# Kernel optimization log

Hardware: AMD Instinct MI355X
Metric: run time of the kernel (lower is better)

## Reference

```python
import jax, jax.numpy as jnp
import numpy as np

B, S, D, H, L, V = 2, 1024, 1024, 16, 8, 50257
HD = D // H
FF = 4 * D
EPS = 1e-5


def setup_inputs() -> dict:
    key = jax.random.key(0)
    ks = jax.random.split(key, 16)
    s = 0.02
    return {
        "idx": jax.random.randint(ks[0], (B, S), 0, V, dtype=jnp.int32),
        "tok_emb": jax.random.normal(ks[1], (V, D), jnp.float32) * s,
        "pos_emb": jax.random.normal(ks[2], (S, D), jnp.float32) * s,
        "qkv_w": jax.random.normal(ks[3], (L, 3 * D, D), jnp.float32) * s,
        "proj_w": jax.random.normal(ks[4], (L, D, D), jnp.float32) * s,
        "proj_b": jnp.zeros((L, D), jnp.float32),
        "ln1_s": jnp.ones((L, D), jnp.float32),
        "ln1_b": jnp.zeros((L, D), jnp.float32),
        "fc1_w": jax.random.normal(ks[5], (L, FF, D), jnp.float32) * s,
        "fc1_b": jnp.zeros((L, FF), jnp.float32),
        "fc2_w": jax.random.normal(ks[6], (L, D, FF), jnp.float32) * s,
        "fc2_b": jnp.zeros((L, D), jnp.float32),
        "ln2_s": jnp.ones((L, D), jnp.float32),
        "ln2_b": jnp.zeros((L, D), jnp.float32),
        "lnf_s": jnp.ones((D,), jnp.float32),
        "lnf_b": jnp.zeros((D,), jnp.float32),
        "head_w": jax.random.normal(ks[7], (V, D), jnp.float32) * s,
        "head_b": jnp.zeros((V,), jnp.float32),
    }


def _layer_norm(x, scale, bias):
    mu = jnp.mean(x, axis=-1, keepdims=True)
    var = jnp.mean(jnp.square(x - mu), axis=-1, keepdims=True)
    return (x - mu) * jax.lax.rsqrt(var + EPS) * scale + bias


def _attention(x, qkv_w, proj_w, proj_b, causal):
    b, s, d = x.shape
    qkv = jnp.einsum("bsd,ed->bse", x, qkv_w)            # [B,S,3D]
    qkv = qkv.reshape(b, s, H, 3 * HD)                    # per-head interleaved q,k,v
    q, k, v = jnp.split(qkv, 3, axis=-1)                  # each [B,S,H,HD]
    scale = HD ** -0.5
    scores = jnp.einsum("bqhd,bkhd->bhqk", q, k) * scale  # [B,H,S,S]
    scores = jnp.where(causal, scores, -jnp.inf)
    probs = jax.nn.softmax(scores, axis=-1)
    out = jnp.einsum("bhqk,bkhd->bqhd", probs, v).reshape(b, s, d)
    return out @ proj_w.T + proj_b


def reference(idx, tok_emb, pos_emb, qkv_w, proj_w, proj_b, ln1_s, ln1_b,
              fc1_w, fc1_b, fc2_w, fc2_b, ln2_s, ln2_b, lnf_s, lnf_b,
              head_w, head_b):
    s = idx.shape[1]
    causal = jnp.tril(jnp.ones((s, s), dtype=bool))
    x = tok_emb[idx] + pos_emb[None, :s]                  # [B,S,D]
    for l in range(L):
        h = _layer_norm(x, ln1_s[l], ln1_b[l])
        x = x + _attention(h, qkv_w[l], proj_w[l], proj_b[l], causal)
        h = _layer_norm(x, ln2_s[l], ln2_b[l])
        h = jax.nn.relu(h @ fc1_w[l].T + fc1_b[l]) @ fc2_w[l].T + fc2_b[l]
        x = x + h
    x = _layer_norm(x, lnf_s, lnf_b)
    logits = x @ head_w.T + head_b                        # [B,S,V]
    return logits
```

## Files before the change

kernel.cpp:

```cpp
#include <hip/hip_runtime.h>
#include <hip/hip_bf16.h>
#include <math.h>

#define B_  2
#define S_  1024
#define D_  1024
#define H_  16
#define HD_ 64
#define L_  8
#define FF_ 4096
#define V_  50257
#define M_  (B_ * S_)
#define EPS_ 1e-5f

typedef __attribute__((ext_vector_type(8))) short short8;
typedef __attribute__((ext_vector_type(4))) float f32x4;

__device__ __forceinline__ unsigned short f2bf(float f) {
  union { float f; uint32_t u; } c; c.f = f;
  uint32_t r = (c.u + 0x7FFFu + ((c.u >> 16) & 1u)) >> 16;
  return (unsigned short)r;
}
__device__ __forceinline__ void gll16(const unsigned short* g, unsigned short* lds) {
  __builtin_amdgcn_global_load_lds(
      (const __attribute__((address_space(1))) void*)g,
      (__attribute__((address_space(3))) void*)lds, 16, 0, 0);
}

__global__ __launch_bounds__(256) void embed_kernel(
    const int* __restrict__ idx, const float* __restrict__ tok,
    const float* __restrict__ pos, float* __restrict__ x) {
  int i = blockIdx.x * 256 + threadIdx.x;
  int m = i >> 8;
  int d4 = i & 255;
  int s = m & (S_ - 1);
  int t = idx[m];
  float4 tv = ((const float4*)(tok + (size_t)t * D_))[d4];
  float4 pv = ((const float4*)(pos + (size_t)s * D_))[d4];
  float4 o;
  o.x = tv.x + pv.x; o.y = tv.y + pv.y; o.z = tv.z + pv.z; o.w = tv.w + pv.w;
  ((float4*)(x + (size_t)m * D_))[d4] = o;
}

__global__ __launch_bounds__(256) void cvt_bf16_kernel(
    const float* __restrict__ in, unsigned short* __restrict__ out, int n4) {
  int i = blockIdx.x * 256 + threadIdx.x;
  int stride = gridDim.x * 256;
  for (; i < n4; i += stride) {
    float4 v = ((const float4*)in)[i];
    ushort4 o;
    o.x = f2bf(v.x); o.y = f2bf(v.y); o.z = f2bf(v.z); o.w = f2bf(v.w);
    ((ushort4*)out)[i] = o;
  }
}

__global__ __launch_bounds__(256) void cvt4_kernel(
    const float* __restrict__ s0, const float* __restrict__ s1,
    const float* __restrict__ s2, const float* __restrict__ s3,
    unsigned short* __restrict__ d0, unsigned short* __restrict__ d1,
    unsigned short* __restrict__ d2, unsigned short* __restrict__ d3,
    int n0, int n1, int n2, int n3) {
  int total = n0 + n1 + n2 + n3;
  for (int i = blockIdx.x * 256 + threadIdx.x; i < total; i += gridDim.x * 256) {
    const float* s; unsigned short* d; int j = i;
    if (j < n0)              { s = s0; d = d0; }
    else if ((j -= n0) < n1) { s = s1; d = d1; }
    else if ((j -= n1) < n2) { s = s2; d = d2; }
    else                     { j -= n2; s = s3; d = d3; }
    float4 v = ((const float4*)s)[j];
    ushort4 o;
    o.x = f2bf(v.x); o.y = f2bf(v.y); o.z = f2bf(v.z); o.w = f2bf(v.w);
    ((ushort4*)d)[j] = o;
  }
}

__device__ __forceinline__ float block_sum256(float v, float* red) {
  #pragma unroll
  for (int o = 32; o > 0; o >>= 1) v += __shfl_xor(v, o);
  int w = threadIdx.x >> 6;
  __syncthreads();
  if ((threadIdx.x & 63) == 0) red[w] = v;
  __syncthreads();
  return red[0] + red[1] + red[2] + red[3];
}

__global__ __launch_bounds__(256) void layernorm_kernel(
    const float* __restrict__ x, const float* __restrict__ sc,
    const float* __restrict__ bi, unsigned short* __restrict__ out) {
  __shared__ float red[4];
  int row = blockIdx.x;
  float4 v = ((const float4*)(x + (size_t)row * D_))[threadIdx.x];
  float sum = block_sum256(v.x + v.y + v.z + v.w, red);
  float mu = sum * (1.0f / D_);
  float dx = v.x - mu, dy = v.y - mu, dz = v.z - mu, dw = v.w - mu;
  float sq = block_sum256(dx*dx + dy*dy + dz*dz + dw*dw, red);
  float r = rsqrtf(sq * (1.0f / D_) + EPS_);
  int c = threadIdx.x * 4;
  float4 s4 = *(const float4*)(sc + c);
  float4 b4 = *(const float4*)(bi + c);
  ushort4 o;
  o.x = f2bf(dx * r * s4.x + b4.x);
  o.y = f2bf(dy * r * s4.y + b4.y);
  o.z = f2bf(dz * r * s4.z + b4.z);
  o.w = f2bf(dw * r * s4.w + b4.w);
  ((ushort4*)(out + (size_t)row * D_))[threadIdx.x] = o;
}

__global__ __launch_bounds__(256) void reduce_ln_kernel(
    const float* __restrict__ parts, const float* __restrict__ bias,
    float* __restrict__ x, const float* __restrict__ sc,
    const float* __restrict__ bi, unsigned short* __restrict__ h) {
  __shared__ float red[4];
  int row = blockIdx.x;
  int i = row * 256 + threadIdx.x;
  float4 v = ((const float4*)x)[i];
  float4 bb = ((const float4*)bias)[threadIdx.x];
  v.x += bb.x; v.y += bb.y; v.z += bb.z; v.w += bb.w;
  #pragma unroll
  for (int z = 0; z < 4; ++z) {
    float4 p = ((const float4*)(parts + (size_t)z * M_ * D_))[i];
    v.x += p.x; v.y += p.y; v.z += p.z; v.w += p.w;
  }
  ((float4*)x)[i] = v;
  float sum = block_sum256(v.x + v.y + v.z + v.w, red);
  float mu = sum * (1.0f / D_);
  float dx = v.x - mu, dy = v.y - mu, dz = v.z - mu, dw = v.w - mu;
  float sq = block_sum256(dx*dx + dy*dy + dz*dz + dw*dw, red);
  float r = rsqrtf(sq * (1.0f / D_) + EPS_);
  int c = threadIdx.x * 4;
  float4 s4 = *(const float4*)(sc + c);
  float4 b4 = *(const float4*)(bi + c);
  ushort4 o;
  o.x = f2bf(dx * r * s4.x + b4.x);
  o.y = f2bf(dy * r * s4.y + b4.y);
  o.z = f2bf(dz * r * s4.z + b4.z);
  o.w = f2bf(dw * r * s4.w + b4.w);
  ((ushort4*)(h + (size_t)row * D_))[threadIdx.x] = o;
}

#define BM 128
#define BN 128
#define BKg 64

template<bool BIAS, bool RELU, bool OUTBF16>
__global__ __launch_bounds__(256) void gemm_mfma(
    const unsigned short* __restrict__ A, const unsigned short* __restrict__ W,
    const float* __restrict__ bias, void* __restrict__ Cout,
    int M, int N, int K, int lda, int ldc, size_t zstride, int nbx) {
  __shared__ unsigned short As[BM * BKg];
  __shared__ unsigned short Bs[BN * BKg];

  int nwg = gridDim.x;
  int bid = blockIdx.x;
  int q = nwg >> 3, r = nwg & 7;
  int xcd = bid & 7, sub = bid >> 3;
  int swz = (xcd < r ? xcd * (q + 1) : r * (q + 1) + (xcd - r) * q) + sub;
  int by = swz / nbx, bx = swz % nbx;
  int bm = by * BM, bn = bx * BN;

  const size_t Koff = (size_t)blockIdx.y * K;
  const unsigned short* Ab = A + Koff;
  const unsigned short* Wb = W + Koff;

  const int tid = threadIdx.x;
  const int l = tid & 63, w = tid >> 6;
  const int wm = (w >> 1) * 64, wn = (w & 1) * 64;
  const int lr = l >> 3;
  const int lc = (l & 7) << 3;

  const unsigned short* asrc[4];
  const unsigned short* bsrc[4];
  unsigned short* adst[4];
  unsigned short* bdst[4];
  #pragma unroll
  for (int i = 0; i < 4; ++i) {
    int rowa = i * 32 + w * 8;
    asrc[i] = Ab + (size_t)(bm + rowa + lr) * lda + lc;
    adst[i] = As + rowa * BKg;
    int gn = bn + rowa + lr; if (gn >= N) gn = N - 1;
    bsrc[i] = Wb + (size_t)gn * lda + lc;
    bdst[i] = Bs + rowa * BKg;
  }

  f32x4 acc[4][4] = {};
  for (int k0 = 0; k0 < K; k0 += BKg) {
    __syncthreads();
    #pragma unroll
    for (int i = 0; i < 4; ++i) {
      gll16(asrc[i] + k0, adst[i]);
      gll16(bsrc[i] + k0, bdst[i]);
    }
    __syncthreads();
    short8 af[2][4], bfr[2][4];
    #pragma unroll
    for (int ks = 0; ks < 2; ++ks)
      #pragma unroll
      for (int i = 0; i < 4; ++i) {
        af[ks][i]  = *(const short8*)(As + (wm + i * 16 + (l & 15)) * BKg + ks * 32 + (l >> 4) * 8);
        bfr[ks][i] = *(const short8*)(Bs + (wn + i * 16 + (l & 15)) * BKg + ks * 32 + (l >> 4) * 8);
      }
    #pragma unroll
    for (int ks = 0; ks < 2; ++ks)
      #pragma unroll
      for (int i = 0; i < 4; ++i)
        #pragma unroll
        for (int j = 0; j < 4; ++j)
          acc[i][j] = __builtin_amdgcn_mfma_f32_16x16x32_bf16(af[ks][i], bfr[ks][j], acc[i][j], 0, 0, 0);
  }

  const size_t zoff = (size_t)blockIdx.y * zstride;
  const int er = (l >> 4) * 4;
  const int ec = l & 15;
  #pragma unroll
  for (int j = 0; j < 4; ++j) {
    int col = bn + wn + j * 16 + ec;
    if (col < N) {
      float bv = BIAS ? bias[col] : 0.f;
      #pragma unroll
      for (int i = 0; i < 4; ++i) {
        #pragma unroll
        for (int rr = 0; rr < 4; ++rr) {
          int row = bm + wm + i * 16 + er + rr;
          float v = acc[i][j][rr] + bv;
          if (RELU) v = fmaxf(v, 0.f);
          if (OUTBF16) ((unsigned short*)Cout + zoff)[(size_t)row * ldc + col] = f2bf(v);
          else         ((float*)Cout + zoff)[(size_t)row * ldc + col] = v;
        }
      }
    }
  }
}

__global__ __launch_bounds__(256) void attn_mfma_kernel(
    const unsigned short* __restrict__ qkv, unsigned short* __restrict__ out) {
  __shared__ unsigned short Kl[128 * 72];
  __shared__ unsigned short Vt[64 * 136];
  __shared__ unsigned short Pl[4 * 16 * 136];
  const int h = blockIdx.y, b = blockIdx.z;
  const int tile = b ? blockIdx.x : (15 - blockIdx.x);
  const int q0 = tile * 64;
  const int nt = (q0 + 191) >> 7;
  const int tid = threadIdx.x;
  const int l = tid & 63, wid = tid >> 6;
  const int g = l >> 4, m15 = l & 15;
  const size_t rs = 3 * D_;
  const unsigned short* base = qkv + (size_t)(b * S_) * rs + h * (3 * HD_);
  const int sd = wid * 16;
  unsigned short* Pw = Pl + wid * 16 * 136;

  const unsigned short* qp = base + (size_t)(q0 + wid * 16 + m15) * rs + g * 8;
  short8 qf0 = *(const short8*)(qp);
  short8 qf1 = *(const short8*)(qp + 32);
  f32x4 acc_o[4] = {};
  float mrun[4] = {-INFINITY, -INFINITY, -INFINITY, -INFINITY};
  float ssum[4] = {0.f, 0.f, 0.f, 0.f};

  short8 kA0, kA1, kB0, kB1, vA0, vA1, vB0, vB1;
  {
    const unsigned short* r0 = base + (size_t)l * rs + HD_ + sd;
    const unsigned short* r1 = r0 + 64 * rs;
    kA0 = *(const short8*)(r0);       kA1 = *(const short8*)(r0 + 8);
    vA0 = *(const short8*)(r0 + HD_); vA1 = *(const short8*)(r0 + HD_ + 8);
    kB0 = *(const short8*)(r1);       kB1 = *(const short8*)(r1 + 8);
    vB0 = *(const short8*)(r1 + HD_); vB1 = *(const short8*)(r1 + HD_ + 8);
  }

  for (int kt = 0; kt < nt; ++kt) {
    const int k128 = kt << 7;
    __syncthreads();
    *(short8*)(Kl + l * 72 + sd) = kA0;
    *(short8*)(Kl + l * 72 + sd + 8) = kA1;
    *(short8*)(Kl + (64 + l) * 72 + sd) = kB0;
    *(short8*)(Kl + (64 + l) * 72 + sd + 8) = kB1;
    #pragma unroll
    for (int e = 0; e < 8; ++e) {
      Vt[(sd + e) * 136 + l] = (unsigned short)vA0[e];
      Vt[(sd + 8 + e) * 136 + l] = (unsigned short)vA1[e];
      Vt[(sd + e) * 136 + 64 + l] = (unsigned short)vB0[e];
      Vt[(sd + 8 + e) * 136 + 64 + l] = (unsigned short)vB1[e];
    }
    __syncthreads();
    if (kt + 1 < nt) {
      const unsigned short* r0 = base + (size_t)(k128 + 128 + l) * rs + HD_ + sd;
      const unsigned short* r1 = r0 + 64 * rs;
      kA0 = *(const short8*)(r0);       kA1 = *(const short8*)(r0 + 8);
      vA0 = *(const short8*)(r0 + HD_); vA1 = *(const short8*)(r0 + HD_ + 8);
      kB0 = *(const short8*)(r1);       kB1 = *(const short8*)(r1 + 8);
      vB0 = *(const short8*)(r1 + HD_); vB1 = *(const short8*)(r1 + HD_ + 8);
    }

    f32x4 sc8[8] = {};
    __builtin_amdgcn_s_setprio(1);
    #pragma unroll
    for (int j = 0; j < 8; ++j) {
      short8 kf0 = *(const short8*)(Kl + (j * 16 + m15) * 72 + g * 8);
      short8 kf1 = *(const short8*)(Kl + (j * 16 + m15) * 72 + 32 + g * 8);
      sc8[j] = __builtin_amdgcn_mfma_f32_16x16x32_bf16(qf0, kf0, sc8[j], 0, 0, 0);
      sc8[j] = __builtin_amdgcn_mfma_f32_16x16x32_bf16(qf1, kf1, sc8[j], 0, 0, 0);
    }
    __builtin_amdgcn_s_setprio(0);

    const bool lastt = (kt == nt - 1);
    #pragma unroll
    for (int rr = 0; rr < 4; ++rr) {
      const int qrow = q0 + wid * 16 + g * 4 + rr;
      float sv[8];
      #pragma unroll
      for (int j = 0; j < 8; ++j) {
        sv[j] = sc8[j][rr] * 0.125f;
        if (lastt && (k128 + j * 16 + m15 > qrow)) sv[j] = -1e30f;
      }
      float mx = sv[0];
      #pragma unroll
      for (int j = 1; j < 8; ++j) mx = fmaxf(mx, sv[j]);
      mx = fmaxf(mx, __shfl_xor(mx, 1));
      mx = fmaxf(mx, __shfl_xor(mx, 2));
      mx = fmaxf(mx, __shfl_xor(mx, 4));
      mx = fmaxf(mx, __shfl_xor(mx, 8));
      float mn = fmaxf(mrun[rr], mx);
      float corr = __expf(mrun[rr] - mn);
      mrun[rr] = mn;
      float ts = 0.f;
      #pragma unroll
      for (int j = 0; j < 8; ++j) {
        float p = __expf(sv[j] - mn);
        ts += p;
        Pw[(g * 4 + rr) * 136 + j * 16 + m15] = f2bf(p);
      }
      ts += __shfl_xor(ts, 1); ts += __shfl_xor(ts, 2);
      ts += __shfl_xor(ts, 4); ts += __shfl_xor(ts, 8);
      ssum[rr] = ssum[rr] * corr + ts;
      #pragma unroll
      for (int j = 0; j < 4; ++j) acc_o[j][rr] *= corr;
    }

    short8 pa[4];
    #pragma unroll
    for (int ks = 0; ks < 4; ++ks)
      pa[ks] = *(const short8*)(Pw + m15 * 136 + ks * 32 + g * 8);
    __builtin_amdgcn_s_setprio(1);
    #pragma unroll
    for (int j = 0; j < 4; ++j) {
      #pragma unroll
      for (int ks = 0; ks < 4; ++ks) {
        short8 vb = *(const short8*)(Vt + (j * 16 + m15) * 136 + ks * 32 + g * 8);
        acc_o[j] = __builtin_amdgcn_mfma_f32_16x16x32_bf16(pa[ks], vb, acc_o[j], 0, 0, 0);
      }
    }
    __builtin_amdgcn_s_setprio(0);
  }

  #pragma unroll
  for (int rr = 0; rr < 4; ++rr) {
    const int qrow = q0 + wid * 16 + g * 4 + rr;
    float inv = 1.0f / ssum[rr];
    #pragma unroll
    for (int j = 0; j < 4; ++j)
      out[(size_t)(b * S_ + qrow) * D_ + h * HD_ + j * 16 + m15] =
          f2bf(acc_o[j][rr] * inv);
  }
}

static inline void cvt(const float* src, unsigned short* dst, size_t n, hipStream_t s) {
  int n4 = (int)(n / 4);
  int blocks = (n4 + 255) / 256;
  if (blocks > 2048) blocks = 2048;
  cvt_bf16_kernel<<<blocks, 256, 0, s>>>(src, dst, n4);
}

extern "C" void kernel_launch(void* const* d_in, const int* in_sizes, int n_in,
                              void* d_out, int out_size, void* d_ws, size_t ws_size,
                              hipStream_t stream) {
  const int*   idx    = (const int*)d_in[0];
  const float* tok    = (const float*)d_in[1];
  const float* pos    = (const float*)d_in[2];
  const float* qkv_w  = (const float*)d_in[3];
  const float* proj_w = (const float*)d_in[4];
  const float* proj_b = (const float*)d_in[5];
  const float* ln1_s  = (const float*)d_in[6];
  const float* ln1_b  = (const float*)d_in[7];
  const float* fc1_w  = (const float*)d_in[8];
  const float* fc1_b  = (const float*)d_in[9];
  const float* fc2_w  = (const float*)d_in[10];
  const float* fc2_b  = (const float*)d_in[11];
  const float* ln2_s  = (const float*)d_in[12];
  const float* ln2_b  = (const float*)d_in[13];
  const float* lnf_s  = (const float*)d_in[14];
  const float* lnf_b  = (const float*)d_in[15];
  const float* head_w = (const float*)d_in[16];
  const float* head_b = (const float*)d_in[17];
  float* out = (float*)d_out;

  char* wsb = (char*)d_ws;
  float*          x      = (float*)(wsb);
  unsigned short* h      = (unsigned short*)(wsb + (8u << 20));
  unsigned short* qkvb   = (unsigned short*)(wsb + (12u << 20));
  unsigned short* attnb  = (unsigned short*)(wsb + (24u << 20));
  unsigned short* ff     = (unsigned short*)(wsb + (28u << 20));
  unsigned short* wq     = (unsigned short*)(wsb + (44u << 20));
  unsigned short* wp     = (unsigned short*)(wsb + (50u << 20));
  unsigned short* w1     = (unsigned short*)(wsb + (52u << 20));
  unsigned short* w2     = (unsigned short*)(wsb + (60u << 20));
  float*          parts  = (float*)(wsb + (68u << 20));
  unsigned short* hw     = (unsigned short*)(wsb + (100u << 20));

  embed_kernel<<<M_ * D_ / 4 / 256, 256, 0, stream>>>(idx, tok, pos, x);
  layernorm_kernel<<<M_, 256, 0, stream>>>(x, ln1_s, ln1_b, h);

  for (int l = 0; l < L_; ++l) {
    cvt4_kernel<<<2048, 256, 0, stream>>>(
        qkv_w + (size_t)l * 3 * D_ * D_, proj_w + (size_t)l * D_ * D_,
        fc1_w + (size_t)l * FF_ * D_, fc2_w + (size_t)l * D_ * FF_,
        wq, wp, w1, w2,
        3 * D_ * D_ / 4, D_ * D_ / 4, FF_ * D_ / 4, D_ * FF_ / 4);
    gemm_mfma<false, false, true><<<dim3(24 * 16, 1), 256, 0, stream>>>(
        h, wq, nullptr, qkvb, M_, 3 * D_, D_, D_, 3 * D_, 0, 24);
    attn_mfma_kernel<<<dim3(16, H_, B_), 256, 0, stream>>>(qkvb, attnb);
    gemm_mfma<false, false, false><<<dim3(8 * 16, 4), 256, 0, stream>>>(
        attnb, wp, nullptr, parts, M_, D_, 256, D_, D_, (size_t)M_ * D_, 8);
    reduce_ln_kernel<<<M_, 256, 0, stream>>>(
        parts, proj_b + l * D_, x, ln2_s + l * D_, ln2_b + l * D_, h);
    gemm_mfma<true, true, true><<<dim3(32 * 16, 1), 256, 0, stream>>>(
        h, w1, fc1_b + l * FF_, ff, M_, FF_, D_, D_, FF_, 0, 32);
    gemm_mfma<false, false, false><<<dim3(8 * 16, 4), 256, 0, stream>>>(
        ff, w2, nullptr, parts, M_, D_, 1024, FF_, D_, (size_t)M_ * D_, 8);
    const float* ns = (l == L_ - 1) ? lnf_s : ln1_s + (l + 1) * D_;
    const float* nb = (l == L_ - 1) ? lnf_b : ln1_b + (l + 1) * D_;
    reduce_ln_kernel<<<M_, 256, 0, stream>>>(
        parts, fc2_b + l * D_, x, ns, nb, h);
  }

  for (int c0 = 0; c0 < V_; c0 += 8192) {
    int nc = V_ - c0 < 8192 ? V_ - c0 : 8192;
    cvt(head_w + (size_t)c0 * D_, hw, (size_t)nc * D_, stream);
    int nbx = (nc + BN - 1) / BN, nby = M_ / BM;
    gemm_mfma<true, false, false><<<dim3(nbx * nby, 1), 256, 0, stream>>>(
        h, hw, head_b + c0, out + c0, M_, nc, D_, D_, V_, 0, nbx);
  }
}
```

Baseline: 1.884 ms.

## Add specialized 256x256 LM-head GEMM kernel and hoist weight conversion out of the layer loop

Replaces the chunked LM-head path, which converted the head weights 8192 rows at a time and ran one generic GEMM per chunk, with a single dedicated 256x256-tile, 512-thread MFMA kernel. That kernel double-buffers LDS through global_load_lds, uses a swizzled LDS layout, interleaves staging with MFMA phases, raises wave priority around the MFMAs, and swizzles block order. The head weights are padded to a multiple of 256 rows with zeros so the kernel needs no bounds checks on loads. All layer weights are converted to bf16 in a few bulk conversions up front instead of once per layer. The cost is a much larger workspace (about 380 MB) and 128 KB of dynamic LDS per block, which relies on 160 KB LDS per CU.

```diff
diff --git a/kernel.cpp b/kernel.cpp
--- a/kernel.cpp
+++ b/kernel.cpp
@@ -10,8 +10,10 @@
 #define L_  8
 #define FF_ 4096
 #define V_  50257
+#define VP_ 50432
 #define M_  (B_ * S_)
 #define EPS_ 1e-5f
+#define NT_ 16
 
 typedef __attribute__((ext_vector_type(8))) short short8;
 typedef __attribute__((ext_vector_type(4))) float f32x4;
@@ -54,24 +56,10 @@
   }
 }
 
-__global__ __launch_bounds__(256) void cvt4_kernel(
-    const float* __restrict__ s0, const float* __restrict__ s1,
-    const float* __restrict__ s2, const float* __restrict__ s3,
-    unsigned short* __restrict__ d0, unsigned short* __restrict__ d1,
-    unsigned short* __restrict__ d2, unsigned short* __restrict__ d3,
-    int n0, int n1, int n2, int n3) {
-  int total = n0 + n1 + n2 + n3;
-  for (int i = blockIdx.x * 256 + threadIdx.x; i < total; i += gridDim.x * 256) {
-    const float* s; unsigned short* d; int j = i;
-    if (j < n0)              { s = s0; d = d0; }
-    else if ((j -= n0) < n1) { s = s1; d = d1; }
-    else if ((j -= n1) < n2) { s = s2; d = d2; }
-    else                     { j -= n2; s = s3; d = d3; }
-    float4 v = ((const float4*)s)[j];
-    ushort4 o;
-    o.x = f2bf(v.x); o.y = f2bf(v.y); o.z = f2bf(v.z); o.w = f2bf(v.w);
-    ((ushort4*)d)[j] = o;
-  }
+__global__ __launch_bounds__(256) void pad_head_kernel(unsigned short* __restrict__ w) {
+  int i = blockIdx.x * 256 + threadIdx.x;
+  ushort4 z; z.x = 0; z.y = 0; z.z = 0; z.w = 0;
+  ((ushort4*)(w + (size_t)V_ * D_))[i] = z;
 }
 
 __device__ __forceinline__ float block_sum256(float v, float* red) {
@@ -229,6 +217,137 @@
       }
     }
   }
+}
+
+__global__ __launch_bounds__(512, 2) void gemm_head_8p(
+    const unsigned short* __restrict__ A, const unsigned short* __restrict__ W,
+    const float* __restrict__ bias, float* __restrict__ C) {
+  extern __shared__ unsigned short lds[];
+
+  const int nbq = 197;
+  int bid = blockIdx.x;
+  int swz = (bid & 7) * nbq + (bid >> 3);
+  const int bm = (swz & 7) * 256;
+  const int bn = (swz >> 3) * 256;
+
+  const int tid = threadIdx.x;
+  const int l = tid & 63;
+  const int wid = tid >> 6;
+  const int wm = wid >> 2, wn = wid & 3;
+  const int m15 = l & 15, g = l >> 4;
+
+  const int srow = tid >> 2;
+  const int scol = ((tid & 3) * 8) ^ (((tid >> 5) & 1) << 4);
+  const unsigned short* Asrc = A + (size_t)(bm + srow) * 1024 + scol;
+  const unsigned short* Bsrc = W + (size_t)(bn + srow) * 1024 + scol;
+  unsigned short* ldsA = lds + tid * 8;
+  unsigned short* ldsB = lds + 16384 + tid * 8;
+
+  const int arow = wm * 128 + m15;
+  const int asw = (g * 8) ^ (((arow >> 3) & 1) << 4);
+  const unsigned short* aRd = lds + arow * 32 + asw;
+  const int brow = wn * 64 + m15;
+  const int bsw = (g * 8) ^ (((brow >> 3) & 1) << 4);
+  const unsigned short* bRd = lds + 16384 + brow * 32 + bsw;
+
+#define STG_(tt, kh, s) do {                                                          \
+    gll16(Asrc + (size_t)(s) * 131072 + (tt) * 64 + (kh) * 32,                        \
+          ldsA + (((tt) & 1) << 15) + ((kh) << 13) + ((s) << 12));                    \
+    gll16(Bsrc + (size_t)(s) * 131072 + (tt) * 64 + (kh) * 32,                        \
+          ldsB + (((tt) & 1) << 15) + ((kh) << 13) + ((s) << 12));                    \
+  } while (0)
+#define BAR_() do { __builtin_amdgcn_s_barrier(); __builtin_amdgcn_sched_barrier(0); } while (0)
+
+  f32x4 acc[8][4] = {};
+
+  STG_(0, 0, 0); STG_(0, 0, 1);
+  STG_(0, 1, 0); STG_(0, 1, 1);
+  STG_(1, 0, 0); STG_(1, 0, 1);
+  asm volatile("s_waitcnt vmcnt(8)" ::: "memory");
+  __builtin_amdgcn_sched_barrier(0);
+  BAR_();
+
+  #pragma unroll 1
+  for (int t = 0; t < NT_; ++t) {
+    const int cur = (t & 1) << 15;
+    short8 a8[8], b2[2];
+    #pragma unroll
+    for (int mr = 0; mr < 8; ++mr) a8[mr] = *(const short8*)(aRd + cur + mr * 512);
+    b2[0] = *(const short8*)(bRd + cur + 0 * 512);
+    b2[1] = *(const short8*)(bRd + cur + 1 * 512);
+    if (t + 1 < NT_) STG_(t + 1, 1, 0);
+    BAR_();
+    __builtin_amdgcn_s_setprio(1);
+    #pragma unroll
+    for (int mr = 0; mr < 8; ++mr) {
+      acc[mr][0] = __builtin_amdgcn_mfma_f32_16x16x32_bf16(a8[mr], b2[0], acc[mr][0], 0, 0, 0);
+      acc[mr][1] = __builtin_amdgcn_mfma_f32_16x16x32_bf16(a8[mr], b2[1], acc[mr][1], 0, 0, 0);
+    }
+    __builtin_amdgcn_s_setprio(0);
+    BAR_();
+    b2[0] = *(const short8*)(bRd + cur + 2 * 512);
+    b2[1] = *(const short8*)(bRd + cur + 3 * 512);
+    if (t + 1 < NT_) STG_(t + 1, 1, 1);
+    BAR_();
+    __builtin_amdgcn_s_setprio(1);
+    #pragma unroll
+    for (int mr = 0; mr < 8; ++mr) {
+      acc[mr][2] = __builtin_amdgcn_mfma_f32_16x16x32_bf16(a8[mr], b2[0], acc[mr][2], 0, 0, 0);
+      acc[mr][3] = __builtin_amdgcn_mfma_f32_16x16x32_bf16(a8[mr], b2[1], acc[mr][3], 0, 0, 0);
+    }
+    __builtin_amdgcn_s_setprio(0);
+    if (t < NT_ - 1) asm volatile("s_waitcnt vmcnt(8)" ::: "memory");
+    else             asm volatile("s_waitcnt vmcnt(0)" ::: "memory");
+    __builtin_amdgcn_sched_barrier(0);
+    BAR_();
+    #pragma unroll
+    for (int mr = 0; mr < 8; ++mr) a8[mr] = *(const short8*)(aRd + cur + 8192 + mr * 512);
+    b2[0] = *(const short8*)(bRd + cur + 8192 + 0 * 512);
+    b2[1] = *(const short8*)(bRd + cur + 8192 + 1 * 512);
+    if (t + 2 < NT_) STG_(t + 2, 0, 0);
+    BAR_();
+    __builtin_amdgcn_s_setprio(1);
+    #pragma unroll
+    for (int mr = 0; mr < 8; ++mr) {
+      acc[mr][0] = __builtin_amdgcn_mfma_f32_16x16x32_bf16(a8[mr], b2[0], acc[mr][0], 0, 0, 0);
+      acc[mr][1] = __builtin_amdgcn_mfma_f32_16x16x32_bf16(a8[mr], b2[1], acc[mr][1], 0, 0, 0);
+    }
+    __builtin_amdgcn_s_setprio(0);
+    BAR_();
+    b2[0] = *(const short8*)(bRd + cur + 8192 + 2 * 512);
+    b2[1] = *(const short8*)(bRd + cur + 8192 + 3 * 512);
+    if (t + 2 < NT_) STG_(t + 2, 0, 1);
+    BAR_();
+    __builtin_amdgcn_s_setprio(1);
+    #pragma unroll
+    for (int mr = 0; mr < 8; ++mr) {
+      acc[mr][2] = __builtin_amdgcn_mfma_f32_16x16x32_bf16(a8[mr], b2[0], acc[mr][2], 0, 0, 0);
+      acc[mr][3] = __builtin_amdgcn_mfma_f32_16x16x32_bf16(a8[mr], b2[1], acc[mr][3], 0, 0, 0);
+    }
+    __builtin_amdgcn_s_setprio(0);
+    if (t < NT_ - 2)       asm volatile("s_waitcnt vmcnt(8)" ::: "memory");
+    else if (t == NT_ - 2) asm volatile("s_waitcnt vmcnt(4)" ::: "memory");
+    __builtin_amdgcn_sched_barrier(0);
+    BAR_();
+  }
+
+  #pragma unroll
+  for (int nr = 0; nr < 4; ++nr) {
+    int col = bn + wn * 64 + nr * 16 + m15;
+    if (col < V_) {
+      float bv = bias[col];
+      #pragma unroll
+      for (int mr = 0; mr < 8; ++mr) {
+        #pragma unroll
+        for (int rr = 0; rr < 4; ++rr) {
+          int row = bm + wm * 128 + mr * 16 + g * 4 + rr;
+          C[(size_t)row * V_ + col] = acc[mr][nr][rr] + bv;
+        }
+      }
+    }
+  }
+#undef STG_
+#undef BAR_
 }
 
 __global__ __launch_bounds__(256) void attn_mfma_kernel(
@@ -397,44 +516,41 @@
   unsigned short* qkvb   = (unsigned short*)(wsb + (12u << 20));
   unsigned short* attnb  = (unsigned short*)(wsb + (24u << 20));
   unsigned short* ff     = (unsigned short*)(wsb + (28u << 20));
-  unsigned short* wq     = (unsigned short*)(wsb + (44u << 20));
-  unsigned short* wp     = (unsigned short*)(wsb + (50u << 20));
-  unsigned short* w1     = (unsigned short*)(wsb + (52u << 20));
-  unsigned short* w2     = (unsigned short*)(wsb + (60u << 20));
-  float*          parts  = (float*)(wsb + (68u << 20));
-  unsigned short* hw     = (unsigned short*)(wsb + (100u << 20));
+  float*          parts  = (float*)(wsb + (44u << 20));
+  unsigned short* wqkv   = (unsigned short*)(wsb + (76u << 20));
+  unsigned short* wproj  = (unsigned short*)(wsb + (127u << 20));
+  unsigned short* wfc1   = (unsigned short*)(wsb + (144u << 20));
+  unsigned short* wfc2   = (unsigned short*)(wsb + (212u << 20));
+  unsigned short* whead  = (unsigned short*)(wsb + (280u << 20));
+
+  cvt(qkv_w, wqkv, (size_t)L_ * 3 * D_ * D_, stream);
+  cvt(proj_w, wproj, (size_t)L_ * D_ * D_, stream);
+  cvt(fc1_w, wfc1, (size_t)L_ * FF_ * D_, stream);
+  cvt(fc2_w, wfc2, (size_t)L_ * D_ * FF_, stream);
+  cvt(head_w, whead, (size_t)V_ * D_, stream);
+  pad_head_kernel<<<175, 256, 0, stream>>>(whead);
 
   embed_kernel<<<M_ * D_ / 4 / 256, 256, 0, stream>>>(idx, tok, pos, x);
   layernorm_kernel<<<M_, 256, 0, stream>>>(x, ln1_s, ln1_b, h);
 
   for (int l = 0; l < L_; ++l) {
-    cvt4_kernel<<<2048, 256, 0, stream>>>(
-        qkv_w + (size_t)l * 3 * D_ * D_, proj_w + (size_t)l * D_ * D_,
-        fc1_w + (size_t)l * FF_ * D_, fc2_w + (size_t)l * D_ * FF_,
-        wq, wp, w1, w2,
-        3 * D_ * D_ / 4, D_ * D_ / 4, FF_ * D_ / 4, D_ * FF_ / 4);
     gemm_mfma<false, false, true><<<dim3(24 * 16, 1), 256, 0, stream>>>(
-        h, wq, nullptr, qkvb, M_, 3 * D_, D_, D_, 3 * D_, 0, 24);
+        h, wqkv + (size_t)l * 3 * D_ * D_, nullptr, qkvb, M_, 3 * D_, D_, D_, 3 * D_, 0, 24);
     attn_mfma_kernel<<<dim3(16, H_, B_), 256, 0, stream>>>(qkvb, attnb);
     gemm_mfma<false, false, false><<<dim3(8 * 16, 4), 256, 0, stream>>>(
-        attnb, wp, nullptr, parts, M_, D_, 256, D_, D_, (size_t)M_ * D_, 8);
+        attnb, wproj + (size_t)l * D_ * D_, nullptr, parts, M_, D_, 256, D_, D_, (size_t)M_ * D_, 8);
     reduce_ln_kernel<<<M_, 256, 0, stream>>>(
         parts, proj_b + l * D_, x, ln2_s + l * D_, ln2_b + l * D_, h);
     gemm_mfma<true, true, true><<<dim3(32 * 16, 1), 256, 0, stream>>>(
-        h, w1, fc1_b + l * FF_, ff, M_, FF_, D_, D_, FF_, 0, 32);
+        h, wfc1 + (size_t)l * FF_ * D_, fc1_b + l * FF_, ff, M_, FF_, D_, D_, FF_, 0, 32);
     gemm_mfma<false, false, false><<<dim3(8 * 16, 4), 256, 0, stream>>>(
-        ff, w2, nullptr, parts, M_, D_, 1024, FF_, D_, (size_t)M_ * D_, 8);
+        ff, wfc2 + (size_t)l * D_ * FF_, nullptr, parts, M_, D_, 1024, FF_, D_, (size_t)M_ * D_, 8);
     const float* ns = (l == L_ - 1) ? lnf_s : ln1_s + (l + 1) * D_;
     const float* nb = (l == L_ - 1) ? lnf_b : ln1_b + (l + 1) * D_;
     reduce_ln_kernel<<<M_, 256, 0, stream>>>(
         parts, fc2_b + l * D_, x, ns, nb, h);
   }
 
-  for (int c0 = 0; c0 < V_; c0 += 8192) {
-    int nc = V_ - c0 < 8192 ? V_ - c0 : 8192;
-    cvt(head_w + (size_t)c0 * D_, hw, (size_t)nc * D_, stream);
-    int nbx = (nc + BN - 1) / BN, nby = M_ / BM;
-    gemm_mfma<true, false, false><<<dim3(nbx * nby, 1), 256, 0, stream>>>(
-        h, hw, head_b + c0, out + c0, M_, nc, D_, D_, V_, 0, nbx);
-  }
-}
+  gemm_head_8p<<<dim3((VP_ / 256) * (M_ / 256)), 512, 131072, stream>>>(
+      h, whead, head_b, out);
+}
```

Result: slower. 1.946 ms (+3.3%).
